# Kernel optimization log

Hardware: AMD Instinct MI355X
Metric: run time of the kernel (lower is better)

Reference implementation:

```python
import jax, jax.numpy as jnp
import numpy as np

IN_DIM, HID, OUT_DIM = 128, 24, 4096
B, K = 16384, 256

def setup_inputs() -> dict:
    key = jax.random.key(0)
    ks = jax.random.split(key, 8)
    x = jax.random.normal(ks[0], (B, IN_DIM), dtype=jnp.float32)
    possible_moves = jax.random.randint(ks[1], (B, K), 0, OUT_DIM)
    s1 = 1.0 / np.sqrt(IN_DIM)
    s2 = 1.0 / np.sqrt(HID)
    W1 = jax.random.uniform(ks[2], (IN_DIM, HID), jnp.float32, -s1, s1)
    b1 = jax.random.uniform(ks[3], (HID,), jnp.float32, -s1, s1)
    W2 = jax.random.uniform(ks[4], (HID, HID), jnp.float32, -s2, s2)
    b2 = jax.random.uniform(ks[5], (HID,), jnp.float32, -s2, s2)
    W3 = jax.random.uniform(ks[6], (HID, OUT_DIM), jnp.float32, -s2, s2)
    b3 = jax.random.uniform(ks[7], (OUT_DIM,), jnp.float32, -s2, s2)
    return {"x": x, "possible_moves": possible_moves,
            "W1": W1, "b1": b1, "W2": W2, "b2": b2, "W3": W3, "b3": b3}

def reference(x, possible_moves, W1, b1, W2, b2, W3, b3):
    # small MLP: 128 -> 24 -> 24 -> 4096
    h = jax.nn.relu(x @ W1 + b1)
    h = jax.nn.relu(h @ W2 + b2)
    logits = h @ W3 + b3                     # [B, OUT_DIM]
    # per-row legal-move mask via vectorized scatter (duplicates just re-set 1)
    Bn = logits.shape[0]
    rows = jnp.arange(Bn)[:, None]           # [B, 1] broadcasts over K
    mask = jnp.zeros_like(logits).at[rows, possible_moves].set(1.0)
    # faithful to original: multiply (not -inf) then softmax over full dim
    filtered = logits * mask
    return jax.nn.softmax(filtered, axis=1)
```

## Files before the change

kernel.cpp:

```cpp
#include <hip/hip_runtime.h>
#include <hip/hip_bf16.h>

#define IN_DIM 128
#define HID 24
#define OUT_DIM 4096
#define NB 16384
#define KMOV 256

__global__ __launch_bounds__(256) void ktranspose(const float* __restrict__ W3,
                                                  float* __restrict__ W3T) {
    int t = blockIdx.x * 256 + threadIdx.x;
    if (t < OUT_DIM * HID) {
        int c = t / HID;
        int k = t - c * HID;
        W3T[t] = W3[k * OUT_DIM + c];
    }
}

__global__ __launch_bounds__(256) void kmlp(const float* __restrict__ x,
                                            const float* __restrict__ W1,
                                            const float* __restrict__ b1,
                                            const float* __restrict__ W2,
                                            const float* __restrict__ b2,
                                            float* __restrict__ h2out) {
    __shared__ float W1s[IN_DIM * HID];
    __shared__ float W2s[HID * HID];
    __shared__ float b1s[HID], b2s[HID];
    __shared__ float xs[8][IN_DIM];

    int t = threadIdx.x;
    for (int i = t; i < IN_DIM * HID; i += 256) W1s[i] = W1[i];
    for (int i = t; i < HID * HID; i += 256)    W2s[i] = W2[i];
    if (t < HID) { b1s[t] = b1[t]; b2s[t] = b2[t]; }
    int rbase = blockIdx.x * 8;
    for (int i = t; i < 8 * IN_DIM; i += 256)
        xs[i >> 7][i & 127] = x[(size_t)rbase * IN_DIM + i];
    __syncthreads();

    int g = t >> 5;
    int j = t & 31;
    int r = rbase + g;

    float h1 = 0.f;
    if (j < HID) {
        h1 = b1s[j];
        #pragma unroll 8
        for (int i = 0; i < IN_DIM; i++) h1 += xs[g][i] * W1s[i * HID + j];
        h1 = fmaxf(h1, 0.f);
    }
    float h2 = (j < HID) ? b2s[j] : 0.f;
    #pragma unroll
    for (int k = 0; k < HID; k++) {
        float hk = __shfl(h1, k, 32);
        if (j < HID) h2 += hk * W2s[k * HID + j];
    }
    if (j < HID) {
        h2 = fmaxf(h2, 0.f);
        h2out[(size_t)r * HID + j] = h2;
    }
}

__global__ __launch_bounds__(256) void kmain(const int* __restrict__ moves,
                                             const float* __restrict__ b3,
                                             const float* __restrict__ W3T,
                                             const float* __restrict__ h2all,
                                             float* __restrict__ out) {
    __shared__ float4 f4[OUT_DIM / 4];
    __shared__ float h2s[HID];
    __shared__ float red[8];

    float* filt = (float*)f4;
    int r = blockIdx.x;
    int t = threadIdx.x;

    float4 z = make_float4(0.f, 0.f, 0.f, 0.f);
    #pragma unroll
    for (int i = 0; i < 4; i++) f4[t + i * 256] = z;
    if (t < HID) h2s[t] = h2all[(size_t)r * HID + t];
    __syncthreads();

    int c = moves[(size_t)r * KMOV + t];
    const float4* w = (const float4*)(W3T + c * HID);
    float4 a0 = w[0], a1 = w[1], a2 = w[2], a3 = w[3], a4 = w[4], a5 = w[5];
    float acc = b3[c];
    acc += a0.x*h2s[0] + a0.y*h2s[1] + a0.z*h2s[2]  + a0.w*h2s[3];
    acc += a1.x*h2s[4] + a1.y*h2s[5] + a1.z*h2s[6]  + a1.w*h2s[7];
    acc += a2.x*h2s[8] + a2.y*h2s[9] + a2.z*h2s[10] + a2.w*h2s[11];
    acc += a3.x*h2s[12]+ a3.y*h2s[13]+ a3.z*h2s[14] + a3.w*h2s[15];
    acc += a4.x*h2s[16]+ a4.y*h2s[17]+ a4.z*h2s[18] + a4.w*h2s[19];
    acc += a5.x*h2s[20]+ a5.y*h2s[21]+ a5.z*h2s[22] + a5.w*h2s[23];
    filt[c] = acc;

    float m = acc;
    #pragma unroll
    for (int off = 32; off > 0; off >>= 1) m = fmaxf(m, __shfl_xor(m, off, 64));
    int wid = t >> 6;
    if ((t & 63) == 0) red[wid] = m;
    __syncthreads();
    float mm = fmaxf(fmaxf(red[0], red[1]), fmaxf(red[2], red[3]));
    mm = fmaxf(mm, 0.f);
    float base_e = expf(-mm);

    float s = 0.f;
    #pragma unroll
    for (int i = 0; i < 4; i++) {
        float4 v = f4[t + i * 256];
        float4 e;
        e.x = (v.x == 0.f) ? base_e : expf(v.x - mm);
        e.y = (v.y == 0.f) ? base_e : expf(v.y - mm);
        e.z = (v.z == 0.f) ? base_e : expf(v.z - mm);
        e.w = (v.w == 0.f) ? base_e : expf(v.w - mm);
        f4[t + i * 256] = e;
        s += e.x + e.y + e.z + e.w;
    }
    #pragma unroll
    for (int off = 32; off > 0; off >>= 1) s += __shfl_xor(s, off, 64);
    if ((t & 63) == 0) red[4 + wid] = s;
    __syncthreads();
    float inv = 1.0f / (red[4] + red[5] + red[6] + red[7]);

    float4* out4 = (float4*)(out + (size_t)r * OUT_DIM);
    #pragma unroll
    for (int i = 0; i < 4; i++) {
        float4 v = f4[t + i * 256];
        v.x *= inv; v.y *= inv; v.z *= inv; v.w *= inv;
        out4[t + i * 256] = v;
    }
}

extern "C" void kernel_launch(void* const* d_in, const int* in_sizes, int n_in,
                              void* d_out, int out_size, void* d_ws, size_t ws_size,
                              hipStream_t stream) {
    const float* x     = (const float*)d_in[0];
    const int*   moves = (const int*)  d_in[1];
    const float* W1    = (const float*)d_in[2];
    const float* b1    = (const float*)d_in[3];
    const float* W2    = (const float*)d_in[4];
    const float* b2    = (const float*)d_in[5];
    const float* W3    = (const float*)d_in[6];
    const float* b3    = (const float*)d_in[7];
    float* out = (float*)d_out;

    float* W3T = (float*)d_ws;
    float* h2  = (float*)((char*)d_ws + OUT_DIM * HID * 4);

    ktranspose<<<(OUT_DIM * HID + 255) / 256, 256, 0, stream>>>(W3, W3T);
    kmlp<<<NB / 8, 256, 0, stream>>>(x, W1, b1, W2, b2, h2);
    kmain<<<NB, 256, 0, stream>>>(moves, b3, W3T, h2, out);
}
```

Measured before the change: 359.0 us.

## Replace dense LDS softmax with constant fill plus sparse legal-move scatter

```diff
diff --git a/kernel.cpp b/kernel.cpp
--- a/kernel.cpp
+++ b/kernel.cpp
@@ -65,21 +65,17 @@
                                              const float* __restrict__ W3T,
                                              const float* __restrict__ h2all,
                                              float* __restrict__ out) {
-    __shared__ float4 f4[OUT_DIM / 4];
+    __shared__ unsigned char claimed[OUT_DIM];
     __shared__ float h2s[HID];
     __shared__ float red[8];
 
-    float* filt = (float*)f4;
     int r = blockIdx.x;
     int t = threadIdx.x;
 
-    float4 z = make_float4(0.f, 0.f, 0.f, 0.f);
-    #pragma unroll
-    for (int i = 0; i < 4; i++) f4[t + i * 256] = z;
     if (t < HID) h2s[t] = h2all[(size_t)r * HID + t];
+    int c = moves[(size_t)r * KMOV + t];
     __syncthreads();
 
-    int c = moves[(size_t)r * KMOV + t];
     const float4* w = (const float4*)(W3T + c * HID);
     float4 a0 = w[0], a1 = w[1], a2 = w[2], a3 = w[3], a4 = w[4], a5 = w[5];
     float acc = b3[c];
@@ -89,7 +85,8 @@
     acc += a3.x*h2s[12]+ a3.y*h2s[13]+ a3.z*h2s[14] + a3.w*h2s[15];
     acc += a4.x*h2s[16]+ a4.y*h2s[17]+ a4.z*h2s[18] + a4.w*h2s[19];
     acc += a5.x*h2s[20]+ a5.y*h2s[21]+ a5.z*h2s[22] + a5.w*h2s[23];
-    filt[c] = acc;
+
+    claimed[c] = (unsigned char)t;
 
     float m = acc;
     #pragma unroll
@@ -97,35 +94,29 @@
     int wid = t >> 6;
     if ((t & 63) == 0) red[wid] = m;
     __syncthreads();
-    float mm = fmaxf(fmaxf(red[0], red[1]), fmaxf(red[2], red[3]));
-    mm = fmaxf(mm, 0.f);
-    float base_e = expf(-mm);
+    float mm = fmaxf(fmaxf(fmaxf(red[0], red[1]), fmaxf(red[2], red[3])), 0.f);
 
-    float s = 0.f;
-    #pragma unroll
-    for (int i = 0; i < 4; i++) {
-        float4 v = f4[t + i * 256];
-        float4 e;
-        e.x = (v.x == 0.f) ? base_e : expf(v.x - mm);
-        e.y = (v.y == 0.f) ? base_e : expf(v.y - mm);
-        e.z = (v.z == 0.f) ? base_e : expf(v.z - mm);
-        e.w = (v.w == 0.f) ? base_e : expf(v.w - mm);
-        f4[t + i * 256] = e;
-        s += e.x + e.y + e.z + e.w;
-    }
+    float e      = __expf(acc - mm);
+    float base_e = __expf(-mm);
+
+    float contrib = (claimed[c] == (unsigned char)t) ? (e - base_e) : 0.f;
+    float s = contrib;
     #pragma unroll
     for (int off = 32; off > 0; off >>= 1) s += __shfl_xor(s, off, 64);
     if ((t & 63) == 0) red[4 + wid] = s;
     __syncthreads();
-    float inv = 1.0f / (red[4] + red[5] + red[6] + red[7]);
+    float denom = (float)OUT_DIM * base_e + (red[4] + red[5] + red[6] + red[7]);
+    float inv = 1.0f / denom;
+    float oc  = base_e * inv;
 
+    float4 ocv = make_float4(oc, oc, oc, oc);
     float4* out4 = (float4*)(out + (size_t)r * OUT_DIM);
     #pragma unroll
-    for (int i = 0; i < 4; i++) {
-        float4 v = f4[t + i * 256];
-        v.x *= inv; v.y *= inv; v.z *= inv; v.w *= inv;
-        out4[t + i * 256] = v;
-    }
+    for (int i = 0; i < 4; i++) out4[t + i * 256] = ocv;
+
+    __syncthreads();
+
+    out[(size_t)r * OUT_DIM + c] = e * inv;
 }
 
 extern "C" void kernel_launch(void* const* d_in, const int* in_sizes, int n_in,
```

New measurement: 365.1 us. No clear change (+1.7%).
